# Kernel optimization log

Measured on AMD Instinct MI355X. Metric: run time of the kernel, lower is better.

## Reference

```python
import jax, jax.numpy as jnp
import numpy as np

N = 100_000      # nodes
E = 20_000       # hyperedges
NNZ = 1_600_000  # pins (node, hyperedge) pairs
D_IN, D_HID, D_OUT = 128, 128, 64
EPS = 1e-5
NEG_SLOPE = 0.01


def _glorot(key, shape):
    fan_in, fan_out = shape
    lim = np.sqrt(6.0 / (fan_in + fan_out)).astype(np.float32)
    return jax.random.uniform(key, shape, jnp.float32, -lim, lim)


def setup_inputs() -> dict:
    key = jax.random.key(0)
    k = jax.random.split(key, 5)
    x = jax.random.normal(k[0], (N, D_IN), jnp.float32)
    node_idx = jax.random.randint(k[1], (NNZ,), 0, N)
    edge_idx = jax.random.randint(k[2], (NNZ,), 0, E)
    hyperedge_index = jnp.stack([node_idx, edge_idx]).astype(jnp.int64)
    return {
        "x": x,
        "hyperedge_index": hyperedge_index,
        "W1": _glorot(k[3], (D_IN, D_HID)),
        "b1": jnp.zeros((D_HID,), jnp.float32),
        "gamma": jnp.ones((D_HID,), jnp.float32),
        "beta": jnp.zeros((D_HID,), jnp.float32),
        "W3": _glorot(k[4], (D_HID, D_OUT)),
        "b3": jnp.zeros((D_OUT,), jnp.float32),
    }


def hypergraph_conv(x, node_idx, edge_idx, W, b):
    """PyG HypergraphConv (no attention, unit hyperedge weights):
    out = D^-1 H B H^T (x W) + b."""
    x = x @ W  # [N, F]
    ones = jnp.ones(node_idx.shape[0], x.dtype)
    Bdeg = jax.ops.segment_sum(ones, edge_idx, num_segments=E)  # hyperedge degree
    Ddeg = jax.ops.segment_sum(ones, node_idx, num_segments=N)  # node degree
    Binv = jnp.where(Bdeg > 0, 1.0 / Bdeg, 0.0)
    Dinv = jnp.where(Ddeg > 0, 1.0 / Ddeg, 0.0)
    # node -> hyperedge aggregation, scaled by B
    m = jax.ops.segment_sum(x[node_idx], edge_idx, num_segments=E) * Binv[:, None]
    # hyperedge -> node aggregation, scaled by D
    out = jax.ops.segment_sum(m[edge_idx], node_idx, num_segments=N) * Dinv[:, None]
    return out + b


def layer_norm(h, gamma, beta):
    mu = jnp.mean(h, axis=-1, keepdims=True)
    var = jnp.mean(jnp.square(h - mu), axis=-1, keepdims=True)
    return (h - mu) * jax.lax.rsqrt(var + EPS) * gamma + beta


def reference(x, hyperedge_index, W1, b1, gamma, beta, W3, b3):
    node_idx = hyperedge_index[0]
    edge_idx = hyperedge_index[1]
    h = hypergraph_conv(x, node_idx, edge_idx, W1, b1)
    h = layer_norm(h, gamma, beta)
    h = jax.nn.leaky_relu(h, NEG_SLOPE)
    # dropout is identity in eval mode
    z = hypergraph_conv(h, node_idx, edge_idx, W3, b3)
    return z
```

## Files before the change

### kernel.cpp

```cpp
#include <hip/hip_runtime.h>
#include <hip/hip_bf16.h>

#define NNODES 100000
#define NEDGES 20000
#define NPINS  1600000

#define EB_SHIFT 6
#define NB_SHIFT 7
#define NB_E ((NEDGES + 63) / 64)
#define NB_N ((NNODES + 127) / 128)
#define NB_TOT (NB_E + NB_N)
#define ECAP 6144
#define NCAP 2560
#define REG_TOTAL (NB_E * ECAP + NB_N * NCAP)

typedef __attribute__((ext_vector_type(8))) short short8;
typedef __attribute__((ext_vector_type(4))) float f32x4;
typedef unsigned int uint;


static __device__ inline float bf_lo(uint u) { return __uint_as_float(u << 16); }
static __device__ inline float bf_hi(uint u) { return __uint_as_float(u & 0xffff0000u); }

static __device__ inline uint pack_bf2(float a, float b) {
    union { __hip_bfloat16 h; unsigned short u; } ua, ub;
    ua.h = __float2bfloat16(a);
    ub.h = __float2bfloat16(b);
    return ((uint)ub.u << 16) | (uint)ua.u;
}


__global__ void bin_scatter(const int* __restrict__ he, int* __restrict__ ccnt,
                            uint* __restrict__ pairs) {
    __shared__ int hcnt[NB_TOT];
    __shared__ int hbase[NB_TOT];
    int tid = threadIdx.x;
    int base = blockIdx.x * 8192;
    for (int j = tid; j < NB_TOT; j += 256) hcnt[j] = 0;
    __syncthreads();
    for (int k = 0; k < 32; k++) {
        int i = base + k * 256 + tid;
        if (i < NPINS) {
            int n = he[i];
            int e = he[NPINS + i];
            atomicAdd(&hcnt[e >> EB_SHIFT], 1);
            atomicAdd(&hcnt[NB_E + (n >> NB_SHIFT)], 1);
        }
    }
    __syncthreads();
    for (int j = tid; j < NB_TOT; j += 256)
        hbase[j] = hcnt[j] ? atomicAdd(&ccnt[j], hcnt[j]) : 0;
    __syncthreads();
    for (int k = 0; k < 32; k++) {
        int i = base + k * 256 + tid;
        if (i < NPINS) {
            int n = he[i];
            int e = he[NPINS + i];
            int be = e >> EB_SHIFT;
            int pe = atomicAdd(&hbase[be], 1);
            if (pe < ECAP)
                pairs[be * ECAP + pe] = ((uint)(e & 63) << 20) | (uint)n;
            int bn = n >> NB_SHIFT;
            int pn = atomicAdd(&hbase[NB_E + bn], 1);
            if (pn < NCAP)
                pairs[NB_E * ECAP + bn * NCAP + pn] = ((uint)(n & 127) << 20) | (uint)e;
        }
    }
}

template <int KPB, int CAP>
__global__ void bucket_place(const uint* __restrict__ pairs, int regbase,
                             const int* __restrict__ ccnt, int cbase, int kfine_base, int nkeys,
                             int* __restrict__ off, int* __restrict__ cnt,
                             int* __restrict__ pins) {
    constexpr int NIT = CAP / 256;
    __shared__ int fh[KPB];
    __shared__ int fo[KPB];
    __shared__ int fcur[KPB];
    int b = blockIdx.x;
    int tid = threadIdx.x;
    int rb = regbase + b * CAP;
    int count = ccnt[cbase + b];
    if (count > CAP) count = CAP;
    int keyfirst = b * KPB;
    uint pr[NIT];
    for (int k = tid; k < KPB; k += 256) { fh[k] = 0; fcur[k] = 0; }
#pragma unroll
    for (int i = 0; i < NIT; i++) {
        int idx = tid + i * 256;
        if (idx < count) pr[i] = pairs[rb + idx];
    }
    __syncthreads();
#pragma unroll
    for (int i = 0; i < NIT; i++) {
        int idx = tid + i * 256;
        if (idx < count) atomicAdd(&fh[pr[i] >> 20], 1);
    }
    __syncthreads();
    if (tid == 0) {
        int run = rb;
        for (int k = 0; k < KPB; k++) { fo[k] = run; run += fh[k]; }
    }
    __syncthreads();
    for (int k = tid; k < KPB; k += 256) {
        int key = keyfirst + k;
        if (key < nkeys) { off[kfine_base + key] = fo[k]; cnt[kfine_base + key] = fh[k]; }
    }
#pragma unroll
    for (int i = 0; i < NIT; i++) {
        int idx = tid + i * 256;
        if (idx < count) {
            uint p = pr[i];
            int kl = (int)(p >> 20);
            int pos = atomicAdd(&fcur[kl], 1);
            pins[fo[kl] + pos] = (int)(p & 0xFFFFFu);
        }
    }
}


template <int COLS, bool BF16IN>
__global__ void gemm_mfma(const void* __restrict__ Xv, const float* __restrict__ W,
                          unsigned short* __restrict__ Yb) {
    __shared__ __align__(16) char lds[128 * 256 + COLS * 256];
    char* Xl = lds;
    char* Wt = lds + 128 * 256;
    int tid = threadIdx.x;
    long rowbase = (long)blockIdx.x * 128;

    if constexpr (!BF16IN) {
        const float4* X4 = reinterpret_cast<const float4*>(Xv);
#pragma unroll
        for (int i = 0; i < 16; i++) {
            int f = tid + i * 256;
            int r = f >> 5;
            int c4 = f & 31;
            long gr = rowbase + r;
            if (gr > NNODES - 1) gr = NNODES - 1;
            float4 v = X4[gr * 32 + c4];
            uint lo = pack_bf2(v.x, v.y);
            uint hi = pack_bf2(v.z, v.w);
            int byte = r * 256 + ((c4 * 8) ^ ((r & 7) << 4));
            *reinterpret_cast<uint2*>(Xl + byte) = make_uint2(lo, hi);
        }
    } else {
        const uint4* X4 = reinterpret_cast<const uint4*>(Xv);
#pragma unroll
        for (int i = 0; i < 8; i++) {
            int f = tid + i * 256;
            int r = f >> 4;
            int c = f & 15;
            long gr = rowbase + r;
            if (gr > NNODES - 1) gr = NNODES - 1;
            uint4 v = X4[gr * 16 + c];
            int byte = r * 256 + ((c * 16) ^ ((r & 7) << 4));
            *reinterpret_cast<uint4*>(Xl + byte) = v;
        }
    }
    for (int f = tid; f < 128 * COLS / 4; f += 256) {
        int k = f / (COLS / 4);
        int c4 = f % (COLS / 4);
        float4 v = reinterpret_cast<const float4*>(W)[f];
        float vv[4] = {v.x, v.y, v.z, v.w};
#pragma unroll
        for (int j = 0; j < 4; j++) {
            int c = c4 * 4 + j;
            union { __hip_bfloat16 h; short s; } u;
            u.h = __float2bfloat16(vv[j]);
            int byte = c * 256 + ((k * 2) ^ ((c & 7) << 4));
            *reinterpret_cast<short*>(Wt + byte) = u.s;
        }
    }
    __syncthreads();

    constexpr int NF = COLS / 16;
    int wave = tid >> 6;
    int lane = tid & 63;
    int lrow = lane & 15;
    int lq = lane >> 4;
    f32x4 acc[2][NF] = {};

#pragma unroll
    for (int ks = 0; ks < 4; ks++) {
        short8 a[2];
#pragma unroll
        for (int rt = 0; rt < 2; rt++) {
            int r = wave * 32 + rt * 16 + lrow;
            int byte = r * 256 + ((ks * 64 + lq * 16) ^ ((r & 7) << 4));
            a[rt] = *reinterpret_cast<const short8*>(Xl + byte);
        }
#pragma unroll
        for (int nf = 0; nf < NF; nf++) {
            int c = nf * 16 + lrow;
            int byte = c * 256 + ((ks * 64 + lq * 16) ^ ((c & 7) << 4));
            short8 b = *reinterpret_cast<const short8*>(Wt + byte);
            acc[0][nf] = __builtin_amdgcn_mfma_f32_16x16x32_bf16(a[0], b, acc[0][nf], 0, 0, 0);
            acc[1][nf] = __builtin_amdgcn_mfma_f32_16x16x32_bf16(a[1], b, acc[1][nf], 0, 0, 0);
        }
    }

#pragma unroll
    for (int rt = 0; rt < 2; rt++)
#pragma unroll
        for (int nf = 0; nf < NF; nf++)
#pragma unroll
            for (int r = 0; r < 4; r++) {
                long row = rowbase + wave * 32 + rt * 16 + lq * 4 + r;
                if (row < NNODES) {
                    union { __hip_bfloat16 h; unsigned short u; } u;
                    u.h = __float2bfloat16(acc[rt][nf][r]);
                    Yb[row * COLS + nf * 16 + lrow] = u.u;
                }
            }
}


#define ACC_U2(u) do { \
    a0 += bf_lo((u).x); a1 += bf_hi((u).x); a2 += bf_lo((u).y); a3 += bf_hi((u).y); } while (0)

__global__ void edge_agg_128(const uint2* __restrict__ feat2, const int* __restrict__ pins,
                             const int* __restrict__ off, const int* __restrict__ cnt,
                             uint2* __restrict__ outp) {
    int s = blockIdx.x * 4 + (threadIdx.x >> 6);
    if (s >= NEDGES) return;
    int lane = threadIdx.x & 63;
    int half = lane >> 5, fp = lane & 31;
    int start = off[s], c = cnt[s];
    float a0 = 0.f, a1 = 0.f, a2 = 0.f, a3 = 0.f;
    for (int cb = 0; cb < c; cb += 64) {
        int rem = c - cb;
        int lim = rem < 64 ? rem : 64;
        int pk = 0;
        if (lane < lim) pk = pins[start + cb + lane];
        int i = 0;
        for (; i + 8 <= lim; i += 8) {
            int pa = __shfl(pk, i + half);
            int pb = __shfl(pk, i + 2 + half);
            int pc = __shfl(pk, i + 4 + half);
            int pd = __shfl(pk, i + 6 + half);
            uint2 ua = feat2[(uint)pa * 32 + fp];
            uint2 ub = feat2[(uint)pb * 32 + fp];
            uint2 uc = feat2[(uint)pc * 32 + fp];
            uint2 ud = feat2[(uint)pd * 32 + fp];
            ACC_U2(ua); ACC_U2(ub); ACC_U2(uc); ACC_U2(ud);
        }
        for (; i + 2 <= lim; i += 2) {
            int p = __shfl(pk, i + half);
            uint2 u = feat2[(uint)p * 32 + fp];
            ACC_U2(u);
        }
        if (i < lim) {
            int p = __shfl(pk, i);
            if (half == 0) {
                uint2 u = feat2[(uint)p * 32 + fp];
                ACC_U2(u);
            }
        }
    }
    a0 += __shfl_xor(a0, 32); a1 += __shfl_xor(a1, 32);
    a2 += __shfl_xor(a2, 32); a3 += __shfl_xor(a3, 32);
    if (half == 0) {
        float inv = (c > 0) ? (1.f / (float)c) : 0.f;
        outp[(uint)s * 32 + fp] = make_uint2(pack_bf2(a0 * inv, a1 * inv),
                                             pack_bf2(a2 * inv, a3 * inv));
    }
}

__global__ void node_agg_ln(const uint2* __restrict__ m2, const int* __restrict__ pins,
                            const int* __restrict__ off, const int* __restrict__ cnt,
                            const float* __restrict__ b1, const float* __restrict__ gamma,
                            const float* __restrict__ beta, uint2* __restrict__ hout) {
    int s = blockIdx.x * 4 + (threadIdx.x >> 6);
    if (s >= NNODES) return;
    int lane = threadIdx.x & 63;
    int half = lane >> 5, fp = lane & 31;
    int start = off[s], c = cnt[s];
    float a0 = 0.f, a1 = 0.f, a2 = 0.f, a3 = 0.f;
    for (int cb = 0; cb < c; cb += 64) {
        int rem = c - cb;
        int lim = rem < 64 ? rem : 64;
        int pk = 0;
        if (lane < lim) pk = pins[start + cb + lane];
        int i = 0;
        for (; i + 8 <= lim; i += 8) {
            int pa = __shfl(pk, i + half);
            int pb = __shfl(pk, i + 2 + half);
            int pc = __shfl(pk, i + 4 + half);
            int pd = __shfl(pk, i + 6 + half);
            uint2 ua = m2[(uint)pa * 32 + fp];
            uint2 ub = m2[(uint)pb * 32 + fp];
            uint2 uc = m2[(uint)pc * 32 + fp];
            uint2 ud = m2[(uint)pd * 32 + fp];
            ACC_U2(ua); ACC_U2(ub); ACC_U2(uc); ACC_U2(ud);
        }
        for (; i + 2 <= lim; i += 2) {
            int p = __shfl(pk, i + half);
            uint2 u = m2[(uint)p * 32 + fp];
            ACC_U2(u);
        }
        if (i < lim) {
            int p = __shfl(pk, i);
            if (half == 0) {
                uint2 u = m2[(uint)p * 32 + fp];
                ACC_U2(u);
            }
        }
    }
    a0 += __shfl_xor(a0, 32); a1 += __shfl_xor(a1, 32);
    a2 += __shfl_xor(a2, 32); a3 += __shfl_xor(a3, 32);
    float dinv = (c > 0) ? (1.f / (float)c) : 0.f;
    float4 bb = reinterpret_cast<const float4*>(b1)[fp];
    float v0 = a0 * dinv + bb.x;
    float v1 = a1 * dinv + bb.y;
    float v2 = a2 * dinv + bb.z;
    float v3 = a3 * dinv + bb.w;
    float sum = (v0 + v1) + (v2 + v3);
    float sq = (v0 * v0 + v1 * v1) + (v2 * v2 + v3 * v3);
#pragma unroll
    for (int o = 1; o < 32; o <<= 1) {
        sum += __shfl_xor(sum, o);
        sq  += __shfl_xor(sq, o);
    }
    float mu = sum * (1.f / 128.f);
    float var = sq * (1.f / 128.f) - mu * mu;
    float rstd = rsqrtf(var + 1e-5f);
    float4 g  = reinterpret_cast<const float4*>(gamma)[fp];
    float4 be = reinterpret_cast<const float4*>(beta)[fp];
    float h0 = (v0 - mu) * rstd * g.x + be.x;
    float h1 = (v1 - mu) * rstd * g.y + be.y;
    float h2 = (v2 - mu) * rstd * g.z + be.z;
    float h3 = (v3 - mu) * rstd * g.w + be.w;
    h0 = (h0 > 0.f) ? h0 : 0.01f * h0;
    h1 = (h1 > 0.f) ? h1 : 0.01f * h1;
    h2 = (h2 > 0.f) ? h2 : 0.01f * h2;
    h3 = (h3 > 0.f) ? h3 : 0.01f * h3;
    if (half == 0)
        hout[(uint)s * 32 + fp] = make_uint2(pack_bf2(h0, h1), pack_bf2(h2, h3));
}

__global__ void edge_agg_64(const uint2* __restrict__ feat2, const int* __restrict__ pins,
                            const int* __restrict__ off, const int* __restrict__ cnt,
                            uint2* __restrict__ outp) {
    int s = blockIdx.x * 4 + (threadIdx.x >> 6);
    if (s >= NEDGES) return;
    int lane = threadIdx.x & 63;
    int q = lane >> 4, fp = lane & 15;
    int start = off[s], c = cnt[s];
    float a0 = 0.f, a1 = 0.f, a2 = 0.f, a3 = 0.f;
    for (int cb = 0; cb < c; cb += 64) {
        int rem = c - cb;
        int lim = rem < 64 ? rem : 64;
        int pk = 0;
        if (lane < lim) pk = pins[start + cb + lane];
        int i = 0;
        for (; i + 16 <= lim; i += 16) {
            int pa = __shfl(pk, i + q);
            int pb = __shfl(pk, i + 4 + q);
            int pc = __shfl(pk, i + 8 + q);
            int pd = __shfl(pk, i + 12 + q);
            uint2 ua = feat2[(uint)pa * 16 + fp];
            uint2 ub = feat2[(uint)pb * 16 + fp];
            uint2 uc = feat2[(uint)pc * 16 + fp];
            uint2 ud = feat2[(uint)pd * 16 + fp];
            ACC_U2(ua); ACC_U2(ub); ACC_U2(uc); ACC_U2(ud);
        }
        for (; i + 4 <= lim; i += 4) {
            int p = __shfl(pk, i + q);
            uint2 u = feat2[(uint)p * 16 + fp];
            ACC_U2(u);
        }
        if (i < lim) {
            int idx = i + q;
            int p = __shfl(pk, idx < lim ? idx : i);
            if (idx < lim) {
                uint2 u = feat2[(uint)p * 16 + fp];
                ACC_U2(u);
            }
        }
    }
    a0 += __shfl_xor(a0, 16); a1 += __shfl_xor(a1, 16);
    a2 += __shfl_xor(a2, 16); a3 += __shfl_xor(a3, 16);
    a0 += __shfl_xor(a0, 32); a1 += __shfl_xor(a1, 32);
    a2 += __shfl_xor(a2, 32); a3 += __shfl_xor(a3, 32);
    if (lane < 16) {
        float inv = (c > 0) ? (1.f / (float)c) : 0.f;
        outp[(uint)s * 16 + fp] = make_uint2(pack_bf2(a0 * inv, a1 * inv),
                                             pack_bf2(a2 * inv, a3 * inv));
    }
}

__global__ void node_agg_out(const uint2* __restrict__ m2, const int* __restrict__ pins,
                             const int* __restrict__ off, const int* __restrict__ cnt,
                             const float* __restrict__ b3, float4* __restrict__ out4) {
    int s = blockIdx.x * 4 + (threadIdx.x >> 6);
    if (s >= NNODES) return;
    int lane = threadIdx.x & 63;
    int q = lane >> 4, fp = lane & 15;
    int start = off[s], c = cnt[s];
    float a0 = 0.f, a1 = 0.f, a2 = 0.f, a3 = 0.f;
    for (int cb = 0; cb < c; cb += 64) {
        int rem = c - cb;
        int lim = rem < 64 ? rem : 64;
        int pk = 0;
        if (lane < lim) pk = pins[start + cb + lane];
        int i = 0;
        for (; i + 16 <= lim; i += 16) {
            int pa = __shfl(pk, i + q);
            int pb = __shfl(pk, i + 4 + q);
            int pc = __shfl(pk, i + 8 + q);
            int pd = __shfl(pk, i + 12 + q);
            uint2 ua = m2[(uint)pa * 16 + fp];
            uint2 ub = m2[(uint)pb * 16 + fp];
            uint2 uc = m2[(uint)pc * 16 + fp];
            uint2 ud = m2[(uint)pd * 16 + fp];
            ACC_U2(ua); ACC_U2(ub); ACC_U2(uc); ACC_U2(ud);
        }
        for (; i + 4 <= lim; i += 4) {
            int p = __shfl(pk, i + q);
            uint2 u = m2[(uint)p * 16 + fp];
            ACC_U2(u);
        }
        if (i < lim) {
            int idx = i + q;
            int p = __shfl(pk, idx < lim ? idx : i);
            if (idx < lim) {
                uint2 u = m2[(uint)p * 16 + fp];
                ACC_U2(u);
            }
        }
    }
    a0 += __shfl_xor(a0, 16); a1 += __shfl_xor(a1, 16);
    a2 += __shfl_xor(a2, 16); a3 += __shfl_xor(a3, 16);
    a0 += __shfl_xor(a0, 32); a1 += __shfl_xor(a1, 32);
    a2 += __shfl_xor(a2, 32); a3 += __shfl_xor(a3, 32);
    if (lane < 16) {
        float inv = (c > 0) ? (1.f / (float)c) : 0.f;
        float4 bb = reinterpret_cast<const float4*>(b3)[fp];
        out4[(uint)s * 16 + fp] = make_float4(a0 * inv + bb.x, a1 * inv + bb.y,
                                              a2 * inv + bb.z, a3 * inv + bb.w);
    }
}


extern "C" void kernel_launch(void* const* d_in, const int* in_sizes, int n_in,
                              void* d_out, int out_size, void* d_ws, size_t ws_size,
                              hipStream_t stream) {
    const float* x     = (const float*)d_in[0];
    const int*   he    = (const int*)d_in[1];
    const float* W1    = (const float*)d_in[2];
    const float* b1    = (const float*)d_in[3];
    const float* gamma = (const float*)d_in[4];
    const float* beta  = (const float*)d_in[5];
    const float* W3    = (const float*)d_in[6];
    const float* b3    = (const float*)d_in[7];
    float* out = (float*)d_out;

    char* ws = (char*)d_ws;
    uint* xWb = (uint*)ws;
    uint* mb  = (uint*)(ws + 25600000);
    uint* hb  = (uint*)(ws + 25600000 + 5120000);
    char* ip  = ws + 25600000 + 5120000 + 25600000;
    int* off  = (int*)ip;
    int* cnt  = off + (NEDGES + NNODES);
    int* ccnt = cnt + (NEDGES + NNODES);
    int* pins = ccnt + NB_TOT + 64;
    uint* pairs = (uint*)ws;

    const int nblkA = (NPINS + 8191) / 8192;
    const int ngemm = (NNODES + 127) / 128;

    hipMemsetAsync(ccnt, 0, sizeof(int) * NB_TOT, stream);
    bin_scatter<<<nblkA, 256, 0, stream>>>(he, ccnt, pairs);
    bucket_place<64, ECAP><<<NB_E, 256, 0, stream>>>(pairs, 0, ccnt, 0, 0, NEDGES,
                                                     off, cnt, pins);
    bucket_place<128, NCAP><<<NB_N, 256, 0, stream>>>(pairs, NB_E * ECAP, ccnt, NB_E,
                                                      NEDGES, NNODES, off, cnt, pins);

    gemm_mfma<128, false><<<ngemm, 256, 0, stream>>>(x, W1, (unsigned short*)xWb);
    edge_agg_128<<<(NEDGES + 3) / 4, 256, 0, stream>>>((const uint2*)xWb, pins, off, cnt,
                                                       (uint2*)mb);
    node_agg_ln<<<(NNODES + 3) / 4, 256, 0, stream>>>((const uint2*)mb, pins, off + NEDGES,
                                                      cnt + NEDGES, b1, gamma, beta, (uint2*)hb);
    gemm_mfma<64, true><<<ngemm, 256, 0, stream>>>(hb, W3, (unsigned short*)xWb);
    edge_agg_64<<<(NEDGES + 3) / 4, 256, 0, stream>>>((const uint2*)xWb, pins, off, cnt,
                                                      (uint2*)mb);
    node_agg_out<<<(NNODES + 3) / 4, 256, 0, stream>>>((const uint2*)mb, pins, off + NEDGES,
                                                       cnt + NEDGES, b3, (float4*)out);
}
```

Measured before the change: 289.3 us.

## Split node aggregation into two feature-half passes plus separate LayerNorm kernel

Replaces the fused node aggregation plus LayerNorm kernel with two passes, each gathering half of the 128 bf16 features for four pins per wave, writing fp32 pre-norm values to a temporary buffer. A third kernel then applies LayerNorm and leaky ReLU and writes the bf16 output. The aim is to shrink the per-pass gather working set of the edge-message table so it fits better in cache and to fill more lanes per gather. In exchange, the pins lists are read twice, there are extra kernel launches, and a 51 MB fp32 temporary is written and read back.

Result: slower. 324.8 us (+12.2%).

```diff
diff --git a/kernel.cpp b/kernel.cpp
--- a/kernel.cpp
+++ b/kernel.cpp
@@ -266,14 +266,14 @@
     }
 }
 
-__global__ void node_agg_ln(const uint2* __restrict__ m2, const int* __restrict__ pins,
-                            const int* __restrict__ off, const int* __restrict__ cnt,
-                            const float* __restrict__ b1, const float* __restrict__ gamma,
-                            const float* __restrict__ beta, uint2* __restrict__ hout) {
+template <int PHASE>
+__global__ void node_agg_phase(const uint2* __restrict__ mb2, const int* __restrict__ pins,
+                               const int* __restrict__ off, const int* __restrict__ cnt,
+                               const float* __restrict__ b1, float4* __restrict__ vtmp) {
     int s = blockIdx.x * 4 + (threadIdx.x >> 6);
     if (s >= NNODES) return;
     int lane = threadIdx.x & 63;
-    int half = lane >> 5, fp = lane & 31;
+    int q = lane >> 4, fp = lane & 15;
     int start = off[s], c = cnt[s];
     float a0 = 0.f, a1 = 0.f, a2 = 0.f, a3 = 0.f;
     for (int cb = 0; cb < c; cb += 64) {
@@ -282,40 +282,52 @@
         int pk = 0;
         if (lane < lim) pk = pins[start + cb + lane];
         int i = 0;
-        for (; i + 8 <= lim; i += 8) {
-            int pa = __shfl(pk, i + half);
-            int pb = __shfl(pk, i + 2 + half);
-            int pc = __shfl(pk, i + 4 + half);
-            int pd = __shfl(pk, i + 6 + half);
-            uint2 ua = m2[(uint)pa * 32 + fp];
-            uint2 ub = m2[(uint)pb * 32 + fp];
-            uint2 uc = m2[(uint)pc * 32 + fp];
-            uint2 ud = m2[(uint)pd * 32 + fp];
+        for (; i + 16 <= lim; i += 16) {
+            int pa = __shfl(pk, i + q);
+            int pb = __shfl(pk, i + 4 + q);
+            int pc = __shfl(pk, i + 8 + q);
+            int pd = __shfl(pk, i + 12 + q);
+            uint2 ua = mb2[(uint)pa * 32 + PHASE * 16 + fp];
+            uint2 ub = mb2[(uint)pb * 32 + PHASE * 16 + fp];
+            uint2 uc = mb2[(uint)pc * 32 + PHASE * 16 + fp];
+            uint2 ud = mb2[(uint)pd * 32 + PHASE * 16 + fp];
             ACC_U2(ua); ACC_U2(ub); ACC_U2(uc); ACC_U2(ud);
         }
-        for (; i + 2 <= lim; i += 2) {
-            int p = __shfl(pk, i + half);
-            uint2 u = m2[(uint)p * 32 + fp];
+        for (; i + 4 <= lim; i += 4) {
+            int p = __shfl(pk, i + q);
+            uint2 u = mb2[(uint)p * 32 + PHASE * 16 + fp];
             ACC_U2(u);
         }
         if (i < lim) {
-            int p = __shfl(pk, i);
-            if (half == 0) {
-                uint2 u = m2[(uint)p * 32 + fp];
+            int idx = i + q;
+            int p = __shfl(pk, idx < lim ? idx : i);
+            if (idx < lim) {
+                uint2 u = mb2[(uint)p * 32 + PHASE * 16 + fp];
                 ACC_U2(u);
             }
         }
     }
+    a0 += __shfl_xor(a0, 16); a1 += __shfl_xor(a1, 16);
+    a2 += __shfl_xor(a2, 16); a3 += __shfl_xor(a3, 16);
     a0 += __shfl_xor(a0, 32); a1 += __shfl_xor(a1, 32);
     a2 += __shfl_xor(a2, 32); a3 += __shfl_xor(a3, 32);
-    float dinv = (c > 0) ? (1.f / (float)c) : 0.f;
-    float4 bb = reinterpret_cast<const float4*>(b1)[fp];
-    float v0 = a0 * dinv + bb.x;
-    float v1 = a1 * dinv + bb.y;
-    float v2 = a2 * dinv + bb.z;
-    float v3 = a3 * dinv + bb.w;
-    float sum = (v0 + v1) + (v2 + v3);
-    float sq = (v0 * v0 + v1 * v1) + (v2 * v2 + v3 * v3);
+    if (lane < 16) {
+        float dinv = (c > 0) ? (1.f / (float)c) : 0.f;
+        float4 bb = reinterpret_cast<const float4*>(b1)[PHASE * 16 + fp];
+        vtmp[(uint)s * 32 + PHASE * 16 + fp] =
+            make_float4(a0 * dinv + bb.x, a1 * dinv + bb.y,
+                        a2 * dinv + bb.z, a3 * dinv + bb.w);
+    }
+}
+
+__global__ void ln_apply(const float4* __restrict__ vtmp, const float* __restrict__ gamma,
+                         const float* __restrict__ beta, uint2* __restrict__ hout) {
+    int s = blockIdx.x * 8 + (threadIdx.x >> 5);
+    if (s >= NNODES) return;
+    int l = threadIdx.x & 31;
+    float4 v = vtmp[(uint)s * 32 + l];
+    float sum = (v.x + v.y) + (v.z + v.w);
+    float sq = (v.x * v.x + v.y * v.y) + (v.z * v.z + v.w * v.w);
 #pragma unroll
     for (int o = 1; o < 32; o <<= 1) {
         sum += __shfl_xor(sum, o);
@@ -324,18 +336,17 @@
     float mu = sum * (1.f / 128.f);
     float var = sq * (1.f / 128.f) - mu * mu;
     float rstd = rsqrtf(var + 1e-5f);
-    float4 g  = reinterpret_cast<const float4*>(gamma)[fp];
-    float4 be = reinterpret_cast<const float4*>(beta)[fp];
-    float h0 = (v0 - mu) * rstd * g.x + be.x;
-    float h1 = (v1 - mu) * rstd * g.y + be.y;
-    float h2 = (v2 - mu) * rstd * g.z + be.z;
-    float h3 = (v3 - mu) * rstd * g.w + be.w;
+    float4 g  = reinterpret_cast<const float4*>(gamma)[l];
+    float4 be = reinterpret_cast<const float4*>(beta)[l];
+    float h0 = (v.x - mu) * rstd * g.x + be.x;
+    float h1 = (v.y - mu) * rstd * g.y + be.y;
+    float h2 = (v.z - mu) * rstd * g.z + be.z;
+    float h3 = (v.w - mu) * rstd * g.w + be.w;
     h0 = (h0 > 0.f) ? h0 : 0.01f * h0;
     h1 = (h1 > 0.f) ? h1 : 0.01f * h1;
     h2 = (h2 > 0.f) ? h2 : 0.01f * h2;
     h3 = (h3 > 0.f) ? h3 : 0.01f * h3;
-    if (half == 0)
-        hout[(uint)s * 32 + fp] = make_uint2(pack_bf2(h0, h1), pack_bf2(h2, h3));
+    hout[(uint)s * 32 + l] = make_uint2(pack_bf2(h0, h1), pack_bf2(h2, h3));
 }
 
 __global__ void edge_agg_64(const uint2* __restrict__ feat2, const int* __restrict__ pins,
@@ -464,6 +475,7 @@
     int* cnt  = off + (NEDGES + NNODES);
     int* ccnt = cnt + (NEDGES + NNODES);
     int* pins = ccnt + NB_TOT + 64;
+    float4* vtmp = (float4*)(ws + 73000000);
     uint* pairs = (uint*)ws;
 
     const int nblkA = (NPINS + 8191) / 8192;
@@ -479,8 +491,14 @@
     gemm_mfma<128, false><<<ngemm, 256, 0, stream>>>(x, W1, (unsigned short*)xWb);
     edge_agg_128<<<(NEDGES + 3) / 4, 256, 0, stream>>>((const uint2*)xWb, pins, off, cnt,
                                                        (uint2*)mb);
-    node_agg_ln<<<(NNODES + 3) / 4, 256, 0, stream>>>((const uint2*)mb, pins, off + NEDGES,
-                                                      cnt + NEDGES, b1, gamma, beta, (uint2*)hb);
+    node_agg_phase<0><<<(NNODES + 3) / 4, 256, 0, stream>>>((const uint2*)mb, pins,
+                                                            off + NEDGES, cnt + NEDGES,
+                                                            b1, vtmp);
+    node_agg_phase<1><<<(NNODES + 3) / 4, 256, 0, stream>>>((const uint2*)mb, pins,
+                                                            off + NEDGES, cnt + NEDGES,
+                                                            b1, vtmp);
+    ln_apply<<<(NNODES + 7) / 8, 256, 0, stream>>>(vtmp, gamma, beta, (uint2*)hb);
+
     gemm_mfma<64, true><<<ngemm, 256, 0, stream>>>(hb, W3, (unsigned short*)xWb);
     edge_agg_64<<<(NEDGES + 3) / 4, 256, 0, stream>>>((const uint2*)xWb, pins, off, cnt,
                                                       (uint2*)mb);
```
